# Performance work log

Hardware: AMD Instinct MI355X
Metric: run time of the kernel (lower is better)

Reference implementation:

```python
import jax, jax.numpy as jnp
import numpy as np

EMBED_DIM = 4
SEQ_LEN = 14 * 14


def setup_inputs() -> dict:
    key = jax.random.key(0)
    ks = jax.random.split(key, 7)
    B = 32768
    x = jax.random.normal(ks[0], (B, 1, 28, 28), dtype=jnp.float32)
    conv_w = jax.random.normal(ks[1], (4, 1, 2, 2), dtype=jnp.float32) * 0.5
    conv_b = jax.random.normal(ks[2], (4,), dtype=jnp.float32) * 0.1
    rotation_params = jax.random.uniform(ks[3], (16,), dtype=jnp.float32)
    entangle_params = jax.random.uniform(ks[4], (16,), dtype=jnp.float32)
    lin_w = jax.random.normal(ks[5], (10, 784), dtype=jnp.float32) * 0.05
    lin_b = jax.random.normal(ks[6], (10,), dtype=jnp.float32) * 0.05
    return {"x": x, "conv_w": conv_w, "conv_b": conv_b,
            "rotation_params": rotation_params, "entangle_params": entangle_params,
            "lin_w": lin_w, "lin_b": lin_b}


def reference(x, conv_w, conv_b, rotation_params, entangle_params, lin_w, lin_b):
    B = x.shape[0]
    # Quanvolution filter: Conv2d(1,4,k=2,s=2) -> [B,4,14,14]
    feat = jax.lax.conv_general_dilated(
        x, conv_w, window_strides=(2, 2), padding='VALID',
        dimension_numbers=('NCHW', 'OIHW', 'NCHW'))
    feat = feat + conv_b[None, :, None, None]
    # flatten (channel-major like torch .view) then reshape to [B, 196, 4]
    feat = feat.reshape(B, -1).reshape(B, SEQ_LEN, EMBED_DIM)
    # mean embedding per sample: [B, 4]
    mean_embeds = feat.mean(axis=1)
    # classical self-attention on a length-1 sequence per sample
    R = rotation_params.reshape(EMBED_DIM, EMBED_DIM)
    E = entangle_params.reshape(EMBED_DIM, EMBED_DIM)
    q = mean_embeds @ R                               # [B, 4]
    k = mean_embeds @ E                               # [B, 4]
    scores = jnp.einsum('bd,bd->b', q, k) / jnp.sqrt(jnp.float32(EMBED_DIM))
    # softmax over a single-element axis (seq_len == 1) -> all ones, kept for fidelity
    scores = jax.nn.softmax(scores[:, None], axis=-1)  # [B, 1]
    attn_weights = scores * mean_embeds                # [B, 4] (== mean_embeds)
    # broadcast-scale features and classify
    feat = (feat * attn_weights[:, None, :]).reshape(B, -1)  # [B, 784]
    logits = feat @ lin_w.T + lin_b
    return jax.nn.log_softmax(logits, axis=-1)
```

## Files before the change

### kernel.cpp

```cpp
#include <hip/hip_runtime.h>


typedef __attribute__((ext_vector_type(8))) short bf16x8;
typedef __attribute__((ext_vector_type(4))) float f32x4;
typedef __attribute__((ext_vector_type(4))) unsigned int uint4v;

union BU { uint4v u; bf16x8 b; };

__device__ __forceinline__ unsigned short f2bf(float f) {
  unsigned u = __float_as_uint(f);
  unsigned r = u + 0x7FFFu + ((u >> 16) & 1u);
  return (unsigned short)(r >> 16);
}
__device__ __forceinline__ float bf2f(unsigned short h) {
  return __uint_as_float((unsigned)h << 16);
}

#define CST_F 38400
#define A_F   38440

__global__ void qsac_prep(const float* __restrict__ cw, const float* __restrict__ cb,
                          const float* __restrict__ lw, float* __restrict__ wsf) {
  const int i = blockIdx.x * 256 + threadIdx.x;
  const int e = i & 7, lane = (i >> 3) & 63, c = i >> 9;
  const int t = c / 3, nt = c - t * 3;
  const int nn = lane & 15, kb = lane >> 4;
  const int col = nt * 16 + nn;
  const int k = t * 32 + kb * 8 + e;
  float val = 0.f;
  if (k < 784) {
    const int r = k / 28, cc = k - r * 28;
    const int kh = r & 1, kw = cc & 1;
    const int p = (r >> 1) * 14 + (cc >> 1);
    const int dpix = (2 * ((r >> 1) & 1) + (cc >> 1)) & 3;
    const int cd = col / 12, cj = col - cd * 12;
    if (cd == dpix) {
      const float w0 = cw[(kh << 1) + kw],     w1 = cw[4 + (kh << 1) + kw],
                  w2 = cw[8 + (kh << 1) + kw], w3 = cw[12 + (kh << 1) + kw];
      if (cj < 10)
        val = w0 * lw[cj * 784 + p]       + w1 * lw[cj * 784 + 196 + p] +
              w2 * lw[cj * 784 + 392 + p] + w3 * lw[cj * 784 + 588 + p];
      else if (cj == 10)
        val = (w0 + w1 + w2 + w3) * (1.0f / 196.0f);
    }
  }
  wsf[i] = val;

  if (blockIdx.x == 0) {
    const int u = threadIdx.x;
    if (u < 40) {
      const int d = u / 10, j = u - (u / 10) * 10;
      const float b0 = cb[0], b1 = cb[1], b2 = cb[2], b3 = cb[3];
      float s = 0.f;
#pragma unroll 7
      for (int q = d; q < 196; q += 4)
        s += b0 * lw[j * 784 + q]       + b1 * lw[j * 784 + 196 + q] +
             b2 * lw[j * 784 + 392 + q] + b3 * lw[j * 784 + 588 + q];
      wsf[CST_F + u] = s;
    } else if (u == 40) {
      wsf[A_F] = (cb[0] + cb[1] + cb[2] + cb[3]) * 0.25f;
    }
  }
}

__global__ __launch_bounds__(512)
__attribute__((amdgpu_waves_per_eu(2, 2))) void qsac_main(
    const float* __restrict__ x, const float* __restrict__ wsf,
    const float* __restrict__ lin_b, float* __restrict__ out) {
  __shared__ unsigned int smemu[38400];

  const int tid = threadIdx.x;
  const int lane = tid & 63;
  const int wid = __builtin_amdgcn_readfirstlane(tid >> 6);
  const int nn = lane & 15, kb = lane >> 4;
  const int sbase = blockIdx.x * 128 + wid * 16;
  const float* xrow = x + (size_t)(sbase + nn) * 784;

#pragma unroll
  for (int r = 0; r < 10; ++r) {
    const int j = tid + r * 512;
    if (j < 4800) {
      const float4 f0 = *(const float4*)(wsf + j * 8);
      const float4 f1 = *(const float4*)(wsf + j * 8 + 4);
      const float v[8] = {f0.x, f0.y, f0.z, f0.w, f1.x, f1.y, f1.z, f1.w};
      unsigned short h[8], l[8];
#pragma unroll
      for (int e = 0; e < 8; ++e) {
        h[e] = f2bf(v[e]);
        l[e] = f2bf(v[e] - bf2f(h[e]));
      }
      uint4v hi, lo;
      hi.x = (unsigned)h[0] | ((unsigned)h[1] << 16);
      hi.y = (unsigned)h[2] | ((unsigned)h[3] << 16);
      hi.z = (unsigned)h[4] | ((unsigned)h[5] << 16);
      hi.w = (unsigned)h[6] | ((unsigned)h[7] << 16);
      lo.x = (unsigned)l[0] | ((unsigned)l[1] << 16);
      lo.y = (unsigned)l[2] | ((unsigned)l[3] << 16);
      lo.z = (unsigned)l[4] | ((unsigned)l[5] << 16);
      lo.w = (unsigned)l[6] | ((unsigned)l[7] << 16);
      const int c = j >> 6;
      *(uint4v*)(smemu + c * 512 + lane * 4) = hi;
      *(uint4v*)(smemu + c * 512 + 256 + lane * 4) = lo;
    }
  }
  __syncthreads();

  f32x4 acc[3];
#pragma unroll
  for (int nt = 0; nt < 3; ++nt) acc[nt] = (f32x4){0.f, 0.f, 0.f, 0.f};

  auto ldA = [&](int t, float4& a, float4& b) {
    const int ka = t * 32 + kb * 8;
    const int kc = (ka < 784) ? ka : 0;
    a = *(const float4*)(xrow + kc);
    b = *(const float4*)(xrow + kc + 4);
  };
  auto ldB = [&](int t, BU (&bh)[3], BU (&bl)[3]) {
    const unsigned int* bb = smemu + t * 1536 + lane * 4;
#pragma unroll
    for (int nt = 0; nt < 3; ++nt) {
      bh[nt].u = *(const uint4v*)(bb + nt * 512);
      bl[nt].u = *(const uint4v*)(bb + nt * 512 + 256);
    }
  };
  auto domfma = [&](const float4& a, const float4& b2, BU (&bh)[3], BU (&bl)[3]) {
    const float v[8] = {a.x, a.y, a.z, a.w, b2.x, b2.y, b2.z, b2.w};
    bf16x8 Ah, Al;
#pragma unroll
    for (int e = 0; e < 8; ++e) {
      const unsigned short hh = f2bf(v[e]);
      Ah[e] = (short)hh;
      Al[e] = (short)f2bf(v[e] - bf2f(hh));
    }
#pragma unroll
    for (int nt = 0; nt < 3; ++nt) {
      acc[nt] = __builtin_amdgcn_mfma_f32_16x16x32_bf16(Ah, bh[nt].b, acc[nt], 0, 0, 0);
      acc[nt] = __builtin_amdgcn_mfma_f32_16x16x32_bf16(Al, bh[nt].b, acc[nt], 0, 0, 0);
      acc[nt] = __builtin_amdgcn_mfma_f32_16x16x32_bf16(Ah, bl[nt].b, acc[nt], 0, 0, 0);
    }
  };

  float4 xa0, xb0, xa1, xb1;
  BU bh0[3], bl0[3], bh1[3], bl1[3];
  ldA(0, xa0, xb0);
  ldB(0, bh0, bl0);
#pragma unroll 1
  for (int tt = 0; tt < 12; ++tt) {
    ldA(2 * tt + 1, xa1, xb1);
    ldB(2 * tt + 1, bh1, bl1);
    domfma(xa0, xb0, bh0, bl0);
    ldA(2 * tt + 2, xa0, xb0);
    ldB(2 * tt + 2, bh0, bl0);
    domfma(xa1, xb1, bh1, bl1);
  }
  domfma(xa0, xb0, bh0, bl0);

  __syncthreads();
  float* cx = (float*)smemu + wid * (16 * 52);
#pragma unroll
  for (int nt = 0; nt < 3; ++nt)
#pragma unroll
    for (int rg = 0; rg < 4; ++rg)
      cx[(kb * 4 + rg) * 52 + nt * 16 + nn] = acc[nt][rg];
  __builtin_amdgcn_wave_barrier();

  if (lane < 16) {
    float Y[48];
#pragma unroll
    for (int q = 0; q < 12; ++q) {
      const float4 t4 = *(const float4*)&cx[lane * 52 + q * 4];
      Y[q * 4 + 0] = t4.x; Y[q * 4 + 1] = t4.y;
      Y[q * 4 + 2] = t4.z; Y[q * 4 + 3] = t4.w;
    }
    const float a = wsf[A_F];
    float M[4];
#pragma unroll
    for (int d = 0; d < 4; ++d) M[d] = a + Y[d * 12 + 10];
    float logits[10];
#pragma unroll
    for (int j = 0; j < 10; ++j) {
      float vv = lin_b[j];
#pragma unroll
      for (int d = 0; d < 4; ++d)
        vv += M[d] * (wsf[CST_F + d * 10 + j] + Y[d * 12 + j]);
      logits[j] = vv;
    }
    float mx = logits[0];
#pragma unroll
    for (int j = 1; j < 10; ++j) mx = fmaxf(mx, logits[j]);
    float se = 0.f;
#pragma unroll
    for (int j = 0; j < 10; ++j) se += __expf(logits[j] - mx);
    const float lse = mx + __logf(se);
    float* op = out + (size_t)(sbase + lane) * 10;
#pragma unroll
    for (int j = 0; j < 10; ++j) op[j] = logits[j] - lse;
  }
}

extern "C" void kernel_launch(void* const* d_in, const int* in_sizes, int n_in,
                              void* d_out, int out_size, void* d_ws, size_t ws_size,
                              hipStream_t stream) {
  (void)n_in; (void)ws_size; (void)out_size;
  const float* x = (const float*)d_in[0];
  const float* conv_w = (const float*)d_in[1];
  const float* conv_b = (const float*)d_in[2];
  const float* lin_w = (const float*)d_in[5];
  const float* lin_b = (const float*)d_in[6];
  float* out = (float*)d_out;
  float* wsf = (float*)d_ws;

  hipLaunchKernelGGL(qsac_prep, dim3(150), dim3(256), 0, stream,
                     conv_w, conv_b, lin_w, wsf);

  const int B = in_sizes[0] / 784;
  const int nblk = B / 128;
  hipLaunchKernelGGL(qsac_main, dim3(nblk), dim3(512), 0, stream,
                     x, wsf, lin_b, out);
}
```

Baseline: 31.27 us.

## Pre-split weights to bf16 hi/lo in prep and stream to LDS directly

```diff
diff --git a/kernel.cpp b/kernel.cpp
--- a/kernel.cpp
+++ b/kernel.cpp
@@ -21,12 +21,12 @@
 
 __global__ void qsac_prep(const float* __restrict__ cw, const float* __restrict__ cb,
                           const float* __restrict__ lw, float* __restrict__ wsf) {
+  unsigned short* gt = (unsigned short*)wsf;
   const int i = blockIdx.x * 256 + threadIdx.x;
-  const int e = i & 7, lane = (i >> 3) & 63, c = i >> 9;
+  const int e = i & 7, ln = (i >> 3) & 63, c = i >> 9;
   const int t = c / 3, nt = c - t * 3;
-  const int nn = lane & 15, kb = lane >> 4;
-  const int col = nt * 16 + nn;
-  const int k = t * 32 + kb * 8 + e;
+  const int col = nt * 16 + (ln & 15);
+  const int k = t * 32 + (ln >> 4) * 8 + e;
   float val = 0.f;
   if (k < 784) {
     const int r = k / 28, cc = k - r * 28;
@@ -44,7 +44,9 @@
         val = (w0 + w1 + w2 + w3) * (1.0f / 196.0f);
     }
   }
-  wsf[i] = val;
+  const unsigned short hh = f2bf(val);
+  gt[c * 1024 + ln * 8 + e] = hh;
+  gt[c * 1024 + 512 + ln * 8 + e] = f2bf(val - bf2f(hh));
 
   if (blockIdx.x == 0) {
     const int u = threadIdx.x;
@@ -76,31 +78,24 @@
   const int sbase = blockIdx.x * 128 + wid * 16;
   const float* xrow = x + (size_t)(sbase + nn) * 784;
 
-#pragma unroll
-  for (int r = 0; r < 10; ++r) {
-    const int j = tid + r * 512;
-    if (j < 4800) {
-      const float4 f0 = *(const float4*)(wsf + j * 8);
-      const float4 f1 = *(const float4*)(wsf + j * 8 + 4);
-      const float v[8] = {f0.x, f0.y, f0.z, f0.w, f1.x, f1.y, f1.z, f1.w};
-      unsigned short h[8], l[8];
-#pragma unroll
-      for (int e = 0; e < 8; ++e) {
-        h[e] = f2bf(v[e]);
-        l[e] = f2bf(v[e] - bf2f(h[e]));
-      }
-      uint4v hi, lo;
-      hi.x = (unsigned)h[0] | ((unsigned)h[1] << 16);
-      hi.y = (unsigned)h[2] | ((unsigned)h[3] << 16);
-      hi.z = (unsigned)h[4] | ((unsigned)h[5] << 16);
-      hi.w = (unsigned)h[6] | ((unsigned)h[7] << 16);
-      lo.x = (unsigned)l[0] | ((unsigned)l[1] << 16);
-      lo.y = (unsigned)l[2] | ((unsigned)l[3] << 16);
-      lo.z = (unsigned)l[4] | ((unsigned)l[5] << 16);
-      lo.w = (unsigned)l[6] | ((unsigned)l[7] << 16);
-      const int c = j >> 6;
-      *(uint4v*)(smemu + c * 512 + lane * 4) = hi;
-      *(uint4v*)(smemu + c * 512 + 256 + lane * 4) = lo;
+  {
+    const char* wsb = (const char*)wsf;
+#pragma unroll
+    for (int i = 0; i < 18; ++i) {
+      const int cbase = i * 512 + wid * 64;
+      __builtin_amdgcn_global_load_lds(
+          (const __attribute__((address_space(1))) unsigned int*)
+              (wsb + (size_t)(cbase + lane) * 16),
+          (__attribute__((address_space(3))) unsigned int*)&smemu[cbase * 4],
+          16, 0, 0);
+    }
+    if (wid < 6) {
+      const int cbase = 9216 + wid * 64;
+      __builtin_amdgcn_global_load_lds(
+          (const __attribute__((address_space(1))) unsigned int*)
+              (wsb + (size_t)(cbase + lane) * 16),
+          (__attribute__((address_space(3))) unsigned int*)&smemu[cbase * 4],
+          16, 0, 0);
     }
   }
   __syncthreads();
@@ -109,21 +104,14 @@
 #pragma unroll
   for (int nt = 0; nt < 3; ++nt) acc[nt] = (f32x4){0.f, 0.f, 0.f, 0.f};
 
-  auto ldA = [&](int t, float4& a, float4& b) {
-    const int ka = t * 32 + kb * 8;
-    const int kc = (ka < 784) ? ka : 0;
-    a = *(const float4*)(xrow + kc);
-    b = *(const float4*)(xrow + kc + 4);
-  };
-  auto ldB = [&](int t, BU (&bh)[3], BU (&bl)[3]) {
+  auto tile = [&](const float4& a, const float4& b2, int t) {
+    BU bh[3], bl[3];
     const unsigned int* bb = smemu + t * 1536 + lane * 4;
 #pragma unroll
     for (int nt = 0; nt < 3; ++nt) {
       bh[nt].u = *(const uint4v*)(bb + nt * 512);
       bl[nt].u = *(const uint4v*)(bb + nt * 512 + 256);
     }
-  };
-  auto domfma = [&](const float4& a, const float4& b2, BU (&bh)[3], BU (&bl)[3]) {
     const float v[8] = {a.x, a.y, a.z, a.w, b2.x, b2.y, b2.z, b2.w};
     bf16x8 Ah, Al;
 #pragma unroll
@@ -140,20 +128,26 @@
     }
   };
 
-  float4 xa0, xb0, xa1, xb1;
-  BU bh0[3], bl0[3], bh1[3], bl1[3];
-  ldA(0, xa0, xb0);
-  ldB(0, bh0, bl0);
+#define LD_A(PA, PB, T)                                                       \
+  {                                                                           \
+    const int ka = (T)*32 + kb * 8;                                           \
+    const int kc = (ka < 784) ? ka : 0;      \
+    PA = *(const float4*)(xrow + kc);                                         \
+    PB = *(const float4*)(xrow + kc + 4);                                     \
+  }
+
+  float4 a0, b0, a1, b1, a2, b2, a3, b3;
+  LD_A(a0, b0, 0) LD_A(a1, b1, 1) LD_A(a2, b2, 2) LD_A(a3, b3, 3)
+
 #pragma unroll 1
-  for (int tt = 0; tt < 12; ++tt) {
-    ldA(2 * tt + 1, xa1, xb1);
-    ldB(2 * tt + 1, bh1, bl1);
-    domfma(xa0, xb0, bh0, bl0);
-    ldA(2 * tt + 2, xa0, xb0);
-    ldB(2 * tt + 2, bh0, bl0);
-    domfma(xa1, xb1, bh1, bl1);
-  }
-  domfma(xa0, xb0, bh0, bl0);
+  for (int it = 0; it < 6; ++it) {
+    const int t = it * 4;
+    tile(a0, b0, t + 0); if (t + 4 < 25) LD_A(a0, b0, t + 4)
+    tile(a1, b1, t + 1); if (t + 5 < 25) LD_A(a1, b1, t + 5)
+    tile(a2, b2, t + 2); if (t + 6 < 25) LD_A(a2, b2, t + 6)
+    tile(a3, b3, t + 3); if (t + 7 < 25) LD_A(a3, b3, t + 7)
+  }
+  tile(a0, b0, 24);
 
   __syncthreads();
   float* cx = (float*)smemu + wid * (16 * 52);
@@ -196,6 +190,7 @@
 #pragma unroll
     for (int j = 0; j < 10; ++j) op[j] = logits[j] - lse;
   }
+#undef LD_A
 }
 
 extern "C" void kernel_launch(void* const* d_in, const int* in_sizes, int n_in,
```

After: 30.98 us. Within noise of the previous version (-0.9%).
